# Kernel optimization log

Measured on AMD Instinct MI355X. Metric: run time of the kernel, lower is better.

Reference implementation:

```python
import jax, jax.numpy as jnp
import numpy as np
from jax import lax

B, T, U, V = 4, 200, 100, 1024
D_ENC, D_DEC, J = 144, 320, 320


def setup_inputs() -> dict:
    key = jax.random.key(0)
    ks = jax.random.split(key, 8)
    s = lambda d: 1.0 / np.sqrt(d).astype(np.float32)
    return {
        "enc_out": jax.random.normal(ks[0], (B, T, D_ENC), jnp.float32),
        "dec_out": jax.random.normal(ks[1], (B, U + 1, D_DEC), jnp.float32),
        "W_enc": jax.random.normal(ks[2], (D_ENC, J), jnp.float32) * s(D_ENC),
        "b_enc": jnp.zeros((J,), jnp.float32),
        "W_dec": jax.random.normal(ks[3], (D_DEC, J), jnp.float32) * s(D_DEC),
        "b_dec": jnp.zeros((J,), jnp.float32),
        "W_out": jax.random.normal(ks[4], (J, V), jnp.float32) * s(J),
        "b_out": jnp.zeros((V,), jnp.float32),
        "targets": jax.random.randint(ks[5], (B, U), 1, V, jnp.int32),
        "enc_lengths": jax.random.randint(ks[6], (B,), T // 2, T + 1, jnp.int32),
        "target_lengths": jax.random.randint(ks[7], (B,), U // 2, U + 1, jnp.int32),
    }


def _rnnt_loss(log_probs, targets, enc_lengths, target_lengths):
    # log_probs: [B, T, U+1, V]; blank index = 0 (matches RNNTLoss(blank=0))
    blank_lp = log_probs[..., 0]  # [B, T, U+1]
    idx = jnp.broadcast_to(targets[:, None, :, None].astype(jnp.int32), (B, T, U, 1))
    emit_lp = jnp.take_along_axis(log_probs[:, :, :U, :], idx, axis=-1)[..., 0]  # [B, T, U]

    # alpha[0, u] = sum of emit log-probs along u at t=0
    alpha0 = jnp.concatenate(
        [jnp.zeros((B, 1), log_probs.dtype), jnp.cumsum(emit_lp[:, 0, :], axis=1)], axis=1
    )  # [B, U+1]

    def row(a, emit_t):
        # a: alpha_prev + blank (vertical transitions), [B, U+1]; emit_t: [B, U]
        def step(prev, xs):
            a_u, e_prev = xs
            cur = jnp.logaddexp(a_u, prev + e_prev)
            return cur, cur
        _, rest = lax.scan(step, a[:, 0], (a[:, 1:].T, emit_t.T))  # rest: [U, B]
        return jnp.concatenate([a[:, :1], rest.T], axis=1)

    def t_step(alpha_prev, xs):
        blank_prev, emit_t = xs
        alpha_t = row(alpha_prev + blank_prev, emit_t)
        return alpha_t, alpha_t

    xs = (jnp.swapaxes(blank_lp[:, :-1, :], 0, 1), jnp.swapaxes(emit_lp[:, 1:, :], 0, 1))
    _, alphas_rest = lax.scan(t_step, alpha0, xs)  # [T-1, B, U+1]
    alphas = jnp.concatenate([alpha0[None], alphas_rest], axis=0)  # [T, B, U+1]

    b_idx = jnp.arange(B)
    t_idx = enc_lengths - 1
    ll = alphas[t_idx, b_idx, target_lengths] + blank_lp[b_idx, t_idx, target_lengths]
    return jnp.mean(-ll)  # reduction='mean' over batch


def reference(enc_out, dec_out, W_enc, b_enc, W_dec, b_dec, W_out, b_out, targets, enc_lengths, target_lengths):
    enc_p = enc_out @ W_enc + b_enc  # [B, T, J]
    dec_p = dec_out @ W_dec + b_dec  # [B, U+1, J]
    joint = jnp.tanh(enc_p[:, :, None, :] + dec_p[:, None, :, :])  # [B, T, U+1, J]
    logits = joint @ W_out + b_out  # [B, T, U+1, V]
    log_probs = jax.nn.log_softmax(logits, axis=-1)
    return _rnnt_loss(log_probs, targets, enc_lengths, target_lengths)
```

## Files before the change

kernel.cpp:

```cpp
#include <hip/hip_runtime.h>
#include <hip/hip_bf16.h>
#include <math.h>

#define B_ 4
#define T_ 200
#define U_ 100
#define V_ 1024
#define DE 144
#define DD 320
#define J_ 320
#define M_TOT (B_ * T_ * (U_ + 1))
#define SSTR 328
#define DSTR 104
#define NDIAG 300
#define LOG2E 1.4426950408889634f
#define LN2 0.6931471805599453f

typedef __attribute__((ext_vector_type(8))) short bf16x8_t;
typedef __attribute__((ext_vector_type(4))) float f32x4_t;

__device__ __forceinline__ float fast_tanh(float x) {
    float e = exp2f(x * (2.0f * LOG2E));
    float r = __frcp_rn(e + 1.0f);
    return fmaf(-2.0f, r, 1.0f);
}

__device__ __forceinline__ ushort f2bf(float x) {
    uint u = __float_as_uint(x);
    uint r = (u + 0x7FFFu + ((u >> 16) & 1u)) >> 16;
    return (ushort)r;
}

template <int K>
__device__ __forceinline__ void proj_body(const float* __restrict__ X,
                                          const float* __restrict__ W,
                                          const float* __restrict__ bias,
                                          float* __restrict__ Y,
                                          int r0, int R, float* sx, int tid) {
    constexpr int QK = K / 4;
    for (int q = tid; q < 16 * QK; q += 640) {
        int row = q / QK;
        int kq = q - row * QK;
        int r = r0 + row;
        if (r >= R) r = R - 1;
        *(float4*)&sx[row * K + kq * 4] = *(const float4*)&X[r * K + kq * 4];
    }
    __syncthreads();
    const int half = (tid >= 320) ? 1 : 0;
    const int c = tid - half * 320;
    float acc[8];
#pragma unroll
    for (int i = 0; i < 8; i++) acc[i] = 0.0f;
    for (int k = 0; k < K; k += 4) {
        float w0 = W[(k + 0) * 320 + c];
        float w1 = W[(k + 1) * 320 + c];
        float w2 = W[(k + 2) * 320 + c];
        float w3 = W[(k + 3) * 320 + c];
#pragma unroll
        for (int i = 0; i < 8; i++) {
            const float4 x4 = *(const float4*)&sx[(half * 8 + i) * K + k];
            acc[i] = fmaf(x4.x, w0, acc[i]);
            acc[i] = fmaf(x4.y, w1, acc[i]);
            acc[i] = fmaf(x4.z, w2, acc[i]);
            acc[i] = fmaf(x4.w, w3, acc[i]);
        }
    }
    const float bb = bias[c];
#pragma unroll
    for (int i = 0; i < 8; i++) {
        int r = r0 + half * 8 + i;
        if (r < R) Y[r * 320 + c] = acc[i] + bb;
    }
}

__global__ __launch_bounds__(640) void prep_kernel(
    const float* __restrict__ enc_out, const float* __restrict__ dec_out,
    const float* __restrict__ W_enc, const float* __restrict__ b_enc,
    const float* __restrict__ W_dec, const float* __restrict__ b_dec,
    const float* __restrict__ W_out,
    float* __restrict__ enc_p, float* __restrict__ dec_p,
    ushort* __restrict__ Wt) {
    __shared__ float sx[16 * 320];
    const int bid = blockIdx.x;
    const int tid = threadIdx.x;
    if (bid < 50) {
        proj_body<DE>(enc_out, W_enc, b_enc, enc_p, bid * 16, B_ * T_, sx, tid);
    } else if (bid < 76) {
        proj_body<DD>(dec_out, W_dec, b_dec, dec_p, (bid - 50) * 16,
                      B_ * (U_ + 1), sx, tid);
    } else {
        int idx = (bid - 76) * 640 + tid;
        int k = idx >> 10;
        int v = idx & 1023;
        ushort b = f2bf(W_out[idx]);
        int frag = (v >> 4) * 10 + (k >> 5);
        int lane = (v & 15) | (((k >> 3) & 3) << 4);
        int elem = k & 7;
        Wt[frag * 512 + lane * 8 + elem] = b;
    }
}

__global__ __launch_bounds__(1024, 4) void joint_mfma(
    const float* __restrict__ enc_p, const float* __restrict__ dec_p,
    const ushort* __restrict__ Wt, const float* __restrict__ b_out,
    const int* __restrict__ targets,
    float* __restrict__ bsk, float* __restrict__ esk) {
    __shared__ ushort sh[64 * SSTR];
    __shared__ float parts[16][64];
    __shared__ float lse_sh[64];
    __shared__ int tgt_sh[64];

    const int tid = threadIdx.x;
    const int r0 = blockIdx.x * 64;

    if (tid < 64) {
        int rc = r0 + tid;
        int tg = -1;
        if (rc < M_TOT) {
            int b = rc / 20200;
            int rem = rc - b * 20200;
            int u = rem - (rem / 101) * 101;
            if (u < U_) tg = targets[b * U_ + u];
        }
        tgt_sh[tid] = tg;
    }

    {
        const int si = tid >> 4;
        const int sq = tid & 15;
        int rc = r0 + si;
        if (rc > M_TOT - 1) rc = M_TOT - 1;
        int b = rc / 20200;
        int rem = rc - b * 20200;
        int t = rem / 101;
        int u = rem - t * 101;
        const float4* ep = (const float4*)&enc_p[(b * 200 + t) * 320];
        const float4* dp = (const float4*)&dec_p[(b * 101 + u) * 320];
        ushort* shp = &sh[si * SSTR];
#pragma unroll
        for (int it = 0; it < 5; it++) {
            int kq = sq + it * 16;
            float4 e = ep[kq];
            float4 dd = dp[kq];
            float t0 = fast_tanh(e.x + dd.x);
            float t1 = fast_tanh(e.y + dd.y);
            float t2 = fast_tanh(e.z + dd.z);
            float t3 = fast_tanh(e.w + dd.w);
            __hip_bfloat162 p0 = __float22bfloat162_rn(make_float2(t0, t1));
            __hip_bfloat162 p1 = __float22bfloat162_rn(make_float2(t2, t3));
            uint2 pk;
            pk.x = *(uint*)&p0;
            pk.y = *(uint*)&p1;
            *(uint2*)&shp[kq * 4] = pk;
        }
    }
    __syncthreads();

    const int wave = tid >> 6;
    const int lane = tid & 63;
    const int lrow = lane & 15;
    const int lk = (lane >> 4) * 8;
    const int cb16 = wave * 4;

    f32x4_t acc[4][4];
#pragma unroll
    for (int mt = 0; mt < 4; mt++)
#pragma unroll
        for (int nt = 0; nt < 4; nt++) acc[mt][nt] = (f32x4_t)(0.0f);

    for (int ks = 0; ks < 10; ks++) {
        bf16x8_t a[4];
#pragma unroll
        for (int mt = 0; mt < 4; mt++)
            a[mt] = *(const bf16x8_t*)&sh[(mt * 16 + lrow) * SSTR + ks * 32 + lk];
#pragma unroll
        for (int nt = 0; nt < 4; nt++) {
            bf16x8_t bfr = *(const bf16x8_t*)&Wt[(((cb16 + nt) * 10 + ks) << 9) + lane * 8];
            __builtin_amdgcn_s_setprio(1);
#pragma unroll
            for (int mt = 0; mt < 4; mt++)
                acc[mt][nt] = __builtin_amdgcn_mfma_f32_16x16x32_bf16(a[mt], bfr, acc[mt][nt], 0, 0, 0);
            __builtin_amdgcn_s_setprio(0);
        }
    }

    float bo[4];
#pragma unroll
    for (int nt = 0; nt < 4; nt++) bo[nt] = b_out[wave * 64 + nt * 16 + lrow];
#pragma unroll
    for (int mt = 0; mt < 4; mt++)
#pragma unroll
        for (int nt = 0; nt < 4; nt++) acc[mt][nt] += bo[nt];

#pragma unroll
    for (int mt = 0; mt < 4; mt++) {
#pragma unroll
        for (int j = 0; j < 4; j++) {
            float s = exp2f(acc[mt][0][j] * LOG2E);
            s += exp2f(acc[mt][1][j] * LOG2E);
            s += exp2f(acc[mt][2][j] * LOG2E);
            s += exp2f(acc[mt][3][j] * LOG2E);
#pragma unroll
            for (int off = 1; off < 16; off <<= 1)
                s += __shfl_xor(s, off, 16);
            if (lrow == 0) {
                int row = mt * 16 + (lane >> 4) * 4 + j;
                parts[wave][row] = s;
            }
        }
    }
    __syncthreads();
    if (tid < 64) {
        float s = parts[0][tid];
#pragma unroll
        for (int w = 1; w < 16; w++) s += parts[w][tid];
        lse_sh[tid] = __log2f(s) * LN2;
    }
    __syncthreads();

#pragma unroll
    for (int mt = 0; mt < 4; mt++) {
#pragma unroll
        for (int j = 0; j < 4; j++) {
            int lr = mt * 16 + (lane >> 4) * 4 + j;
            int r = r0 + lr;
            if (r >= M_TOT) continue;
            int tc = tgt_sh[lr];
            bool isblank = (wave == 0) && (lrow == 0);
            bool isemit = (tc >= 0) && ((tc >> 6) == wave) && ((tc & 15) == lrow);
            if (isblank || isemit) {
                int b = r / 20200;
                int rem = r - b * 20200;
                int t = rem / 101;
                int u = rem - t * 101;
                float lse = lse_sh[lr];
                if (isblank)
                    bsk[(b * NDIAG + t + u) * DSTR + u] = acc[mt][0][j] - lse;
                if (isemit) {
                    int ntl = (tc >> 4) & 3;
                    float v = acc[mt][0][j];
#pragma unroll
                    for (int nt = 1; nt < 4; nt++)
                        if (nt == ntl) v = acc[mt][nt][j];
                    esk[(b * NDIAG + t + u) * DSTR + u] = v - lse;
                }
            }
        }
    }
}

__global__ __launch_bounds__(256, 1) void alpha8_kernel(
    const float* __restrict__ bsk, const float* __restrict__ esk,
    const int* __restrict__ enc_len, const int* __restrict__ tgt_len,
    float* __restrict__ out) {
    __shared__ float ll_sh[B_];
    const int tid = threadIdx.x;
    const int b = tid >> 6;
    const int l = tid & 63;
    const float* Bp = bsk + b * (NDIAG * DSTR);
    const float* Ep = esk + b * (NDIAG * DSTR);
    const int el = enc_len[b];
    const int tl = tgt_len[b];
    const int dfin = el - 1 + tl;

    float a1 = (l == 0) ? 0.0f : -INFINITY;
    float a2 = -INFINITY;

    float rb1[8], rb2[8], re1[8], re2[8];
#pragma unroll
    for (int k = 0; k < 8; k++) {
        rb1[k] = Bp[k * DSTR + l];
        rb2[k] = Bp[k * DSTR + 64 + l];
        re1[k] = Ep[k * DSTR + l];
        re2[k] = Ep[k * DSTR + 64 + l];
    }

    for (int dc = 1; dc <= 297; dc += 8) {
#pragma unroll
        for (int q = 0; q < 8; q++) {
            const int d = dc + q;
            if (d > NDIAG - 1) continue;
            const int sc = q;
            const int sm = (q + 1) & 7;
            float cb1 = rb1[sc], cb2 = rb2[sc], ce1 = re1[sc], ce2 = re2[sc];
            float mb1 = rb1[sm], mb2 = rb2[sm];
            int dn = d + 7;
            if (dn > NDIAG - 1) dn = NDIAG - 1;
            rb1[sc] = Bp[dn * DSTR + l];
            rb2[sc] = Bp[dn * DSTR + 64 + l];
            re1[sc] = Ep[dn * DSTR + l];
            re2[sc] = Ep[dn * DSTR + 64 + l];

            float pe1 = __shfl_up(ce1, 1, 64);
            float e1hi = __shfl(ce1, 63, 64);
            float pe2s = __shfl_up(ce2, 1, 64);
            float pe2 = (l == 0) ? e1hi : pe2s;
            float pa1 = __shfl_up(a1, 1, 64);
            float a1hi = __shfl(a1, 63, 64);
            float pa2s = __shfl_up(a2, 1, 64);
            float pa2 = (l == 0) ? a1hi : pa2s;

            const int t1 = d - l;
            float va = a1 + cb1;
            float vb = (l >= 1) ? pa1 + pe1 : -INFINITY;
            float M = fmaxf(va, vb);
            float v1 = (M == -INFINITY)
                           ? -INFINITY
                           : M + __logf(1.0f + __expf(fminf(va, vb) - M));
            if (t1 < 0 || t1 >= T_ || l > U_) v1 = -INFINITY;

            const int t2 = d - 64 - l;
            float va2 = a2 + cb2;
            float vb2 = pa2 + pe2;
            float M2 = fmaxf(va2, vb2);
            float v2 = (M2 == -INFINITY)
                           ? -INFINITY
                           : M2 + __logf(1.0f + __expf(fminf(va2, vb2) - M2));
            if (t2 < 0 || t2 >= T_ || (64 + l) > U_) v2 = -INFINITY;

            if (d == dfin) {
                if (l == tl) ll_sh[b] = v1 + mb1;
                if (64 + l == tl) ll_sh[b] = v2 + mb2;
            }
            a1 = v1;
            a2 = v2;
        }
    }
    __syncthreads();
    if (tid == 0)
        out[0] = -0.25f * (ll_sh[0] + ll_sh[1] + ll_sh[2] + ll_sh[3]);
}

extern "C" void kernel_launch(void* const* d_in, const int* in_sizes, int n_in,
                              void* d_out, int out_size, void* d_ws, size_t ws_size,
                              hipStream_t stream) {
    const float* enc_out = (const float*)d_in[0];
    const float* dec_out = (const float*)d_in[1];
    const float* W_enc = (const float*)d_in[2];
    const float* b_enc = (const float*)d_in[3];
    const float* W_dec = (const float*)d_in[4];
    const float* b_dec = (const float*)d_in[5];
    const float* W_out = (const float*)d_in[6];
    const float* b_out = (const float*)d_in[7];
    const int* targets = (const int*)d_in[8];
    const int* enc_len = (const int*)d_in[9];
    const int* tgt_len = (const int*)d_in[10];

    float* ws = (float*)d_ws;
    float* enc_p = ws;
    float* dec_p = enc_p + B_ * T_ * J_;
    float* bsk = dec_p + B_ * (U_ + 1) * J_;
    float* esk = bsk + B_ * NDIAG * DSTR;
    ushort* Wt = (ushort*)(esk + B_ * NDIAG * DSTR);

    prep_kernel<<<588, 640, 0, stream>>>(enc_out, dec_out, W_enc, b_enc,
                                         W_dec, b_dec, W_out, enc_p, dec_p, Wt);

    joint_mfma<<<(M_TOT + 63) / 64, 1024, 0, stream>>>(
        enc_p, dec_p, Wt, b_out, targets, bsk, esk);

    alpha8_kernel<<<1, 256, 0, stream>>>(bsk, esk, enc_len, tgt_len, (float*)d_out);
}
```

Measured before the change: 213.1 us.

## Make joint MFMA kernel persistent with double-buffered tanh staging and transposed row-sum reduction

```diff
diff --git a/kernel.cpp b/kernel.cpp
--- a/kernel.cpp
+++ b/kernel.cpp
@@ -10,6 +10,7 @@
 #define DD 320
 #define J_ 320
 #define M_TOT (B_ * T_ * (U_ + 1))
+#define NTILES 1263
 #define SSTR 328
 #define DSTR 104
 #define NDIAG 300
@@ -105,30 +106,26 @@
     const ushort* __restrict__ Wt, const float* __restrict__ b_out,
     const int* __restrict__ targets,
     float* __restrict__ bsk, float* __restrict__ esk) {
-    __shared__ ushort sh[64 * SSTR];
+    __shared__ ushort sh[2][64 * SSTR];
     __shared__ float parts[16][64];
     __shared__ float lse_sh[64];
-    __shared__ int tgt_sh[64];
+    __shared__ int tgt_sh[2][64];
 
     const int tid = threadIdx.x;
-    const int r0 = blockIdx.x * 64;
-
-    if (tid < 64) {
-        int rc = r0 + tid;
-        int tg = -1;
-        if (rc < M_TOT) {
-            int b = rc / 20200;
-            int rem = rc - b * 20200;
-            int u = rem - (rem / 101) * 101;
-            if (u < U_) tg = targets[b * U_ + u];
-        }
-        tgt_sh[tid] = tg;
-    }
-
-    {
+    const int wave = tid >> 6;
+    const int lane = tid & 63;
+    const int lrow = lane & 15;
+    const int lk = (lane >> 4) * 8;
+    const int cb16 = wave * 4;
+
+    float bo[4];
+#pragma unroll
+    for (int nt = 0; nt < 4; nt++) bo[nt] = b_out[wave * 64 + nt * 16 + lrow];
+
+    auto stage = [&](int tile, int buf) {
         const int si = tid >> 4;
         const int sq = tid & 15;
-        int rc = r0 + si;
+        int rc = tile * 64 + si;
         if (rc > M_TOT - 1) rc = M_TOT - 1;
         int b = rc / 20200;
         int rem = rc - b * 20200;
@@ -136,7 +133,7 @@
         int u = rem - t * 101;
         const float4* ep = (const float4*)&enc_p[(b * 200 + t) * 320];
         const float4* dp = (const float4*)&dec_p[(b * 101 + u) * 320];
-        ushort* shp = &sh[si * SSTR];
+        ushort* shp = &sh[buf][si * SSTR];
 #pragma unroll
         for (int it = 0; it < 5; it++) {
             int kq = sq + it * 16;
@@ -153,99 +150,141 @@
             pk.y = *(uint*)&p1;
             *(uint2*)&shp[kq * 4] = pk;
         }
-    }
+        if (tid < 64) {
+            int rc2 = tile * 64 + tid;
+            int tg = -1;
+            if (rc2 < M_TOT) {
+                int b2 = rc2 / 20200;
+                int rem2 = rc2 - b2 * 20200;
+                int u2 = rem2 - (rem2 / 101) * 101;
+                if (u2 < U_) tg = targets[b2 * U_ + u2];
+            }
+            tgt_sh[buf][tid] = tg;
+        }
+    };
+
+    stage(blockIdx.x, 0);
     __syncthreads();
 
-    const int wave = tid >> 6;
-    const int lane = tid & 63;
-    const int lrow = lane & 15;
-    const int lk = (lane >> 4) * 8;
-    const int cb16 = wave * 4;
-
-    f32x4_t acc[4][4];
-#pragma unroll
-    for (int mt = 0; mt < 4; mt++)
-#pragma unroll
-        for (int nt = 0; nt < 4; nt++) acc[mt][nt] = (f32x4_t)(0.0f);
-
-    for (int ks = 0; ks < 10; ks++) {
-        bf16x8_t a[4];
+    int cur = 0;
+    for (int tile = blockIdx.x; tile < NTILES; tile += 256) {
+        const int nxt = tile + 256;
+        if (nxt < NTILES) stage(nxt, cur ^ 1);
+
+        f32x4_t acc[4][4];
 #pragma unroll
         for (int mt = 0; mt < 4; mt++)
-            a[mt] = *(const bf16x8_t*)&sh[(mt * 16 + lrow) * SSTR + ks * 32 + lk];
-#pragma unroll
-        for (int nt = 0; nt < 4; nt++) {
-            bf16x8_t bfr = *(const bf16x8_t*)&Wt[(((cb16 + nt) * 10 + ks) << 9) + lane * 8];
-            __builtin_amdgcn_s_setprio(1);
+#pragma unroll
+            for (int nt = 0; nt < 4; nt++) acc[mt][nt] = (f32x4_t)(0.0f);
+
+        const ushort* shc = &sh[cur][0];
+        for (int ks = 0; ks < 10; ks++) {
+            bf16x8_t a[4];
 #pragma unroll
             for (int mt = 0; mt < 4; mt++)
-                acc[mt][nt] = __builtin_amdgcn_mfma_f32_16x16x32_bf16(a[mt], bfr, acc[mt][nt], 0, 0, 0);
-            __builtin_amdgcn_s_setprio(0);
-        }
-    }
-
-    float bo[4];
-#pragma unroll
-    for (int nt = 0; nt < 4; nt++) bo[nt] = b_out[wave * 64 + nt * 16 + lrow];
-#pragma unroll
-    for (int mt = 0; mt < 4; mt++)
-#pragma unroll
-        for (int nt = 0; nt < 4; nt++) acc[mt][nt] += bo[nt];
-
-#pragma unroll
-    for (int mt = 0; mt < 4; mt++) {
-#pragma unroll
-        for (int j = 0; j < 4; j++) {
-            float s = exp2f(acc[mt][0][j] * LOG2E);
-            s += exp2f(acc[mt][1][j] * LOG2E);
-            s += exp2f(acc[mt][2][j] * LOG2E);
-            s += exp2f(acc[mt][3][j] * LOG2E);
-#pragma unroll
-            for (int off = 1; off < 16; off <<= 1)
-                s += __shfl_xor(s, off, 16);
-            if (lrow == 0) {
-                int row = mt * 16 + (lane >> 4) * 4 + j;
-                parts[wave][row] = s;
-            }
-        }
-    }
-    __syncthreads();
-    if (tid < 64) {
-        float s = parts[0][tid];
-#pragma unroll
-        for (int w = 1; w < 16; w++) s += parts[w][tid];
-        lse_sh[tid] = __log2f(s) * LN2;
-    }
-    __syncthreads();
-
-#pragma unroll
-    for (int mt = 0; mt < 4; mt++) {
-#pragma unroll
-        for (int j = 0; j < 4; j++) {
-            int lr = mt * 16 + (lane >> 4) * 4 + j;
-            int r = r0 + lr;
-            if (r >= M_TOT) continue;
-            int tc = tgt_sh[lr];
-            bool isblank = (wave == 0) && (lrow == 0);
-            bool isemit = (tc >= 0) && ((tc >> 6) == wave) && ((tc & 15) == lrow);
-            if (isblank || isemit) {
-                int b = r / 20200;
-                int rem = r - b * 20200;
-                int t = rem / 101;
-                int u = rem - t * 101;
-                float lse = lse_sh[lr];
-                if (isblank)
-                    bsk[(b * NDIAG + t + u) * DSTR + u] = acc[mt][0][j] - lse;
-                if (isemit) {
-                    int ntl = (tc >> 4) & 3;
-                    float v = acc[mt][0][j];
-#pragma unroll
-                    for (int nt = 1; nt < 4; nt++)
-                        if (nt == ntl) v = acc[mt][nt][j];
-                    esk[(b * NDIAG + t + u) * DSTR + u] = v - lse;
+                a[mt] = *(const bf16x8_t*)&shc[(mt * 16 + lrow) * SSTR + ks * 32 + lk];
+#pragma unroll
+            for (int nt = 0; nt < 4; nt++) {
+                bf16x8_t bfr = *(const bf16x8_t*)&Wt[(((cb16 + nt) * 10 + ks) << 9) + lane * 8];
+                __builtin_amdgcn_s_setprio(1);
+#pragma unroll
+                for (int mt = 0; mt < 4; mt++)
+                    acc[mt][nt] = __builtin_amdgcn_mfma_f32_16x16x32_bf16(a[mt], bfr, acc[mt][nt], 0, 0, 0);
+                __builtin_amdgcn_s_setprio(0);
+            }
+        }
+
+#pragma unroll
+        for (int mt = 0; mt < 4; mt++)
+#pragma unroll
+            for (int nt = 0; nt < 4; nt++) acc[mt][nt] += bo[nt];
+
+        float sv[16];
+#pragma unroll
+        for (int mt = 0; mt < 4; mt++)
+#pragma unroll
+            for (int j = 0; j < 4; j++) {
+                float s = exp2f(acc[mt][0][j] * LOG2E);
+                s += exp2f(acc[mt][1][j] * LOG2E);
+                s += exp2f(acc[mt][2][j] * LOG2E);
+                s += exp2f(acc[mt][3][j] * LOG2E);
+                sv[mt * 4 + j] = s;
+            }
+        float v8[8], v4[4], v2[2], vf;
+        {
+            const bool lo1 = (lrow & 1) == 0;
+#pragma unroll
+            for (int i = 0; i < 8; i++) {
+                float send = lo1 ? sv[i + 8] : sv[i];
+                float keep = lo1 ? sv[i] : sv[i + 8];
+                v8[i] = keep + __shfl_xor(send, 1, 64);
+            }
+            const bool lo2 = (lrow & 2) == 0;
+#pragma unroll
+            for (int i = 0; i < 4; i++) {
+                float send = lo2 ? v8[i + 4] : v8[i];
+                float keep = lo2 ? v8[i] : v8[i + 4];
+                v4[i] = keep + __shfl_xor(send, 2, 64);
+            }
+            const bool lo4 = (lrow & 4) == 0;
+#pragma unroll
+            for (int i = 0; i < 2; i++) {
+                float send = lo4 ? v4[i + 2] : v4[i];
+                float keep = lo4 ? v4[i] : v4[i + 2];
+                v2[i] = keep + __shfl_xor(send, 4, 64);
+            }
+            const bool lo8 = (lrow & 8) == 0;
+            float send = lo8 ? v2[1] : v2[0];
+            float keep = lo8 ? v2[0] : v2[1];
+            vf = keep + __shfl_xor(send, 8, 64);
+        }
+        {
+            int slot = ((lrow & 1) << 3) | ((lrow & 2) << 1) |
+                       ((lrow & 4) >> 1) | ((lrow & 8) >> 3);
+            int prow = (slot >> 2) * 16 + (lane >> 4) * 4 + (slot & 3);
+            parts[wave][prow] = vf;
+        }
+        __syncthreads();
+        if (tid < 64) {
+            float s = parts[0][tid];
+#pragma unroll
+            for (int w = 1; w < 16; w++) s += parts[w][tid];
+            lse_sh[tid] = __log2f(s) * LN2;
+        }
+        __syncthreads();
+
+        const int r0 = tile * 64;
+#pragma unroll
+        for (int mt = 0; mt < 4; mt++) {
+#pragma unroll
+            for (int j = 0; j < 4; j++) {
+                int lr = mt * 16 + (lane >> 4) * 4 + j;
+                int r = r0 + lr;
+                if (r >= M_TOT) continue;
+                int tc = tgt_sh[cur][lr];
+                bool isblank = (wave == 0) && (lrow == 0);
+                bool isemit = (tc >= 0) && ((tc >> 6) == wave) && ((tc & 15) == lrow);
+                if (isblank || isemit) {
+                    int b = r / 20200;
+                    int rem = r - b * 20200;
+                    int t = rem / 101;
+                    int u = rem - t * 101;
+                    float lse = lse_sh[lr];
+                    if (isblank)
+                        bsk[(b * NDIAG + t + u) * DSTR + u] = acc[mt][0][j] - lse;
+                    if (isemit) {
+                        int ntl = (tc >> 4) & 3;
+                        float v = acc[mt][0][j];
+#pragma unroll
+                        for (int nt = 1; nt < 4; nt++)
+                            if (nt == ntl) v = acc[mt][nt][j];
+                        esk[(b * NDIAG + t + u) * DSTR + u] = v - lse;
+                    }
                 }
             }
         }
+        __syncthreads();
+        cur ^= 1;
     }
 }
 
@@ -356,7 +395,7 @@
     prep_kernel<<<588, 640, 0, stream>>>(enc_out, dec_out, W_enc, b_enc,
                                          W_dec, b_dec, W_out, enc_p, dec_p, Wt);
 
-    joint_mfma<<<(M_TOT + 63) / 64, 1024, 0, stream>>>(
+    joint_mfma<<<256, 1024, 0, stream>>>(
         enc_p, dec_p, Wt, b_out, targets, bsk, esk);
 
     alpha8_kernel<<<1, 256, 0, stream>>>(bsk, esk, enc_len, tgt_len, (float*)d_out);
```

Result: slower. 314.2 us (+47.4%).

## Remap alpha recursion to two adjacent u per lane and prefetch MFMA B fragments

Applied to the files above, without the earlier changes.

```diff
diff --git a/kernel.cpp b/kernel.cpp
--- a/kernel.cpp
+++ b/kernel.cpp
@@ -168,18 +168,29 @@
 #pragma unroll
         for (int nt = 0; nt < 4; nt++) acc[mt][nt] = (f32x4_t)(0.0f);
 
+    bf16x8_t bnx[4];
+#pragma unroll
+    for (int nt = 0; nt < 4; nt++)
+        bnx[nt] = *(const bf16x8_t*)&Wt[(((cb16 + nt) * 10 + 0) << 9) + lane * 8];
     for (int ks = 0; ks < 10; ks++) {
         bf16x8_t a[4];
 #pragma unroll
         for (int mt = 0; mt < 4; mt++)
             a[mt] = *(const bf16x8_t*)&sh[(mt * 16 + lrow) * SSTR + ks * 32 + lk];
+        bf16x8_t bc[4];
+#pragma unroll
+        for (int nt = 0; nt < 4; nt++) bc[nt] = bnx[nt];
+        if (ks < 9) {
+#pragma unroll
+            for (int nt = 0; nt < 4; nt++)
+                bnx[nt] = *(const bf16x8_t*)&Wt[(((cb16 + nt) * 10 + ks + 1) << 9) + lane * 8];
+        }
 #pragma unroll
         for (int nt = 0; nt < 4; nt++) {
-            bf16x8_t bfr = *(const bf16x8_t*)&Wt[(((cb16 + nt) * 10 + ks) << 9) + lane * 8];
             __builtin_amdgcn_s_setprio(1);
 #pragma unroll
             for (int mt = 0; mt < 4; mt++)
-                acc[mt][nt] = __builtin_amdgcn_mfma_f32_16x16x32_bf16(a[mt], bfr, acc[mt][nt], 0, 0, 0);
+                acc[mt][nt] = __builtin_amdgcn_mfma_f32_16x16x32_bf16(a[mt], bc[nt], acc[mt][nt], 0, 0, 0);
             __builtin_amdgcn_s_setprio(0);
         }
     }
@@ -249,7 +260,7 @@
     }
 }
 
-__global__ __launch_bounds__(256, 1) void alpha8_kernel(
+__global__ __launch_bounds__(256, 1) void alpha_c2_kernel(
     const float* __restrict__ bsk, const float* __restrict__ esk,
     const int* __restrict__ enc_len, const int* __restrict__ tgt_len,
     float* __restrict__ out) {
@@ -263,16 +274,19 @@
     const int tl = tgt_len[b];
     const int dfin = el - 1 + tl;
 
-    float a1 = (l == 0) ? 0.0f : -INFINITY;
-    float a2 = -INFINITY;
-
-    float rb1[8], rb2[8], re1[8], re2[8];
+    const int u0 = 2 * l;
+    const bool ok0 = (u0 <= U_);
+    const bool ok1 = (u0 + 1 <= U_);
+    const int uc = ok0 ? u0 : 0;
+
+    float A0 = (l == 0) ? 0.0f : -INFINITY;
+    float A1 = -INFINITY;
+
+    float2 rb[8], re[8];
 #pragma unroll
     for (int k = 0; k < 8; k++) {
-        rb1[k] = Bp[k * DSTR + l];
-        rb2[k] = Bp[k * DSTR + 64 + l];
-        re1[k] = Ep[k * DSTR + l];
-        re2[k] = Ep[k * DSTR + 64 + l];
+        rb[k] = *(const float2*)&Bp[k * DSTR + uc];
+        re[k] = *(const float2*)&Ep[k * DSTR + uc];
     }
 
     for (int dc = 1; dc <= 297; dc += 8) {
@@ -282,48 +296,40 @@
             if (d > NDIAG - 1) continue;
             const int sc = q;
             const int sm = (q + 1) & 7;
-            float cb1 = rb1[sc], cb2 = rb2[sc], ce1 = re1[sc], ce2 = re2[sc];
-            float mb1 = rb1[sm], mb2 = rb2[sm];
+            float2 cb = rb[sc], ce = re[sc];
+            float2 mb = rb[sm];
             int dn = d + 7;
             if (dn > NDIAG - 1) dn = NDIAG - 1;
-            rb1[sc] = Bp[dn * DSTR + l];
-            rb2[sc] = Bp[dn * DSTR + 64 + l];
-            re1[sc] = Ep[dn * DSTR + l];
-            re2[sc] = Ep[dn * DSTR + 64 + l];
-
-            float pe1 = __shfl_up(ce1, 1, 64);
-            float e1hi = __shfl(ce1, 63, 64);
-            float pe2s = __shfl_up(ce2, 1, 64);
-            float pe2 = (l == 0) ? e1hi : pe2s;
-            float pa1 = __shfl_up(a1, 1, 64);
-            float a1hi = __shfl(a1, 63, 64);
-            float pa2s = __shfl_up(a2, 1, 64);
-            float pa2 = (l == 0) ? a1hi : pa2s;
-
-            const int t1 = d - l;
-            float va = a1 + cb1;
-            float vb = (l >= 1) ? pa1 + pe1 : -INFINITY;
-            float M = fmaxf(va, vb);
-            float v1 = (M == -INFINITY)
+            rb[sc] = *(const float2*)&Bp[dn * DSTR + uc];
+            re[sc] = *(const float2*)&Ep[dn * DSTR + uc];
+
+            float s = A1 + ce.y;
+            float sn = __shfl_up(s, 1, 64);
+
+            float va0 = A0 + cb.x;
+            float vb0 = (l >= 1) ? sn : -INFINITY;
+            float va1 = A1 + cb.y;
+            float vb1 = A0 + ce.x;
+
+            float M0 = fmaxf(va0, vb0);
+            float n0 = (M0 == -INFINITY)
                            ? -INFINITY
-                           : M + __logf(1.0f + __expf(fminf(va, vb) - M));
-            if (t1 < 0 || t1 >= T_ || l > U_) v1 = -INFINITY;
-
-            const int t2 = d - 64 - l;
-            float va2 = a2 + cb2;
-            float vb2 = pa2 + pe2;
-            float M2 = fmaxf(va2, vb2);
-            float v2 = (M2 == -INFINITY)
+                           : M0 + __logf(1.0f + __expf(fminf(va0, vb0) - M0));
+            float M1 = fmaxf(va1, vb1);
+            float n1 = (M1 == -INFINITY)
                            ? -INFINITY
-                           : M2 + __logf(1.0f + __expf(fminf(va2, vb2) - M2));
-            if (t2 < 0 || t2 >= T_ || (64 + l) > U_) v2 = -INFINITY;
+                           : M1 + __logf(1.0f + __expf(fminf(va1, vb1) - M1));
+
+            const int t0 = d - u0;
+            if (!ok0 || t0 < 0 || t0 >= T_) n0 = -INFINITY;
+            if (!ok1 || (t0 - 1) < 0 || (t0 - 1) >= T_) n1 = -INFINITY;
 
             if (d == dfin) {
-                if (l == tl) ll_sh[b] = v1 + mb1;
-                if (64 + l == tl) ll_sh[b] = v2 + mb2;
+                if (tl == u0) ll_sh[b] = n0 + mb.x;
+                if (tl == u0 + 1) ll_sh[b] = n1 + mb.y;
             }
-            a1 = v1;
-            a2 = v2;
+            A0 = n0;
+            A1 = n1;
         }
     }
     __syncthreads();
@@ -359,5 +365,6 @@
     joint_mfma<<<(M_TOT + 63) / 64, 1024, 0, stream>>>(
         enc_p, dec_p, Wt, b_out, targets, bsk, esk);
 
-    alpha8_kernel<<<1, 256, 0, stream>>>(bsk, esk, enc_len, tgt_len, (float*)d_out);
-}
+    alpha_c2_kernel<<<1, 256, 0, stream>>>(bsk, esk, enc_len, tgt_len,
+                                           (float*)d_out);
+}
```

Result: no change. 215.1 us (+0.9%).
